# Performance work log

Hardware: AMD Instinct MI355X
Metric: run time of the kernel (lower is better)

Reference implementation:

```python
import jax, jax.numpy as jnp
import numpy as np

# Fixed problem configuration (regularized ragged structure)
B = 8192      # number of trajectories
D = 32        # input_size
H = 128       # hidden_size
PH = 64       # p_hidden
PREP = 10     # prep_hidden
CS = 8        # cov_size
CH = 32       # cov_hidden
NT = 16       # number of observation times
NO = 4096     # observations per time (trajectories observed)
DT = 0.1      # delta_t (1 euler step between consecutive obs times)
NPOST = 4     # euler steps after last observation up to T
LOGC = float(np.log(np.sqrt(2.0 * np.pi)))


def setup_inputs() -> dict:
    key = jax.random.key(0)
    ks = jax.random.split(key, 24)
    f32 = jnp.float32

    def rn(k, shape, fan_in):
        return jax.random.normal(k, shape, f32) / np.sqrt(fan_in)

    X = jax.random.normal(ks[0], (NT, NO, D), f32)
    M = (jax.random.uniform(ks[1], (NT, NO, D)) < 0.7).astype(f32)  # 0/1 observation mask
    # unique trajectory indices per observation time -> deterministic scatter
    obs_idx = jax.vmap(lambda k: jax.random.permutation(k, B)[:NO])(
        jax.random.split(ks[2], NT)).astype(jnp.int32)
    cov = jax.random.normal(ks[3], (B, CS), f32)

    inp = dict(X=X, M=M, obs_idx=obs_idx, cov=cov)
    # covariates_map: Linear(CS,CH) ReLU Linear(CH,H) Tanh
    inp['cm_w1'] = rn(ks[4], (CS, CH), CS);  inp['cm_b1'] = jnp.zeros((CH,), f32)
    inp['cm_w2'] = rn(ks[5], (CH, H), CH);   inp['cm_b2'] = jnp.zeros((H,), f32)
    # p_model: Linear(H,PH) ReLU Linear(PH,2D)
    inp['p_w1'] = rn(ks[6], (H, PH), H);     inp['p_b1'] = jnp.zeros((PH,), f32)
    inp['p_w2'] = rn(ks[7], (PH, 2 * D), PH); inp['p_b2'] = jnp.zeros((2 * D,), f32)
    # GRUODECell with input 2D
    inp['xz_w'] = rn(ks[8], (2 * D, H), 2 * D); inp['xz_b'] = jnp.zeros((H,), f32)
    inp['hz_w'] = rn(ks[9], (H, H), H)
    inp['xn_w'] = rn(ks[10], (2 * D, H), 2 * D); inp['xn_b'] = jnp.zeros((H,), f32)
    inp['hn_w'] = rn(ks[11], (H, H), H)
    # GRUCell(PREP*D, H): stored as [in, 3H] / [H, 3H], chunk order r,z,n
    inp['w_ih'] = rn(ks[12], (PREP * D, 3 * H), PREP * D)
    inp['w_hh'] = rn(ks[13], (H, 3 * H), H)
    inp['b_ih'] = jnp.zeros((3 * H,), f32)
    inp['b_hh'] = jnp.zeros((3 * H,), f32)
    # observation preprocessing
    std = np.sqrt(2.0 / (4 + PREP))
    inp['w_prep'] = std * jax.random.normal(ks[14], (D, 4, PREP), f32)
    inp['bias_prep'] = 0.1 + jnp.zeros((D, PREP), f32)
    return inp


def reference(X, M, obs_idx, cov,
              cm_w1, cm_b1, cm_w2, cm_b2,
              p_w1, p_b1, p_w2, p_b2,
              xz_w, xz_b, hz_w, xn_w, xn_b, hn_w,
              w_ih, w_hh, b_ih, b_hh, w_prep, bias_prep):
    def p_model(h):
        return jax.nn.relu(h @ p_w1 + p_b1) @ p_w2 + p_b2

    def gru_ode(p, h):  # returns dh/dt as in GRUODECell
        z = jax.nn.sigmoid(p @ xz_w + xz_b + h @ hz_w)
        n = jnp.tanh(p @ xn_w + xn_b + (z * h) @ hn_w)
        return (1.0 - z) * (n - h)

    def gru_cell(x, h):  # torch nn.GRUCell semantics, chunks r,z,n
        gi = x @ w_ih + b_ih
        gh = h @ w_hh + b_hh
        ir, iz, inn = jnp.split(gi, 3, axis=1)
        hr, hz, hn = jnp.split(gh, 3, axis=1)
        r = jax.nn.sigmoid(ir + hr)
        z = jax.nn.sigmoid(iz + hz)
        n = jnp.tanh(inn + r * hn)
        return (1.0 - z) * n + z * h

    h = jnp.tanh(jax.nn.relu(cov @ cm_w1 + cm_b1) @ cm_w2 + cm_b2)  # [B,H]
    p = p_model(h)                                                   # [B,2D]
    loss = jnp.float32(0.0)

    for t in range(NT):
        # one euler ODE step up to the observation time
        h = h + DT * gru_ode(p, h)
        p = p_model(h)
        # Bayesian jump at observed trajectories
        idx = obs_idx[t]            # [NO]
        Xo, Mo = X[t], M[t]         # [NO,D]
        po = p[idx]                 # gather [NO,2D]
        mean, logvar = jnp.split(po, 2, axis=1)
        sigma = jnp.exp(0.5 * logvar)
        err = (Xo - mean) / sigma
        loss = loss + (0.5 * ((err ** 2 + logvar + 2.0 * LOGC) * Mo)).sum()
        feats = jnp.stack([Xo, mean, logvar, err], axis=-1)          # [NO,D,4]
        gin = jax.nn.relu(jnp.einsum('ndf,dfp->ndp', feats, w_prep) + bias_prep)
        gin = (gin * Mo[:, :, None]).reshape(NO, D * PREP)
        h = h.at[idx].set(gru_cell(gin, h[idx]))                     # scatter update
        p = p_model(h)

    for _ in range(NPOST):  # evolve to horizon T
        h = h + DT * gru_ode(p, h)
        p = p_model(h)

    return h, p, loss
```

## Files before the change

kernel.cpp:

```cpp
#include <hip/hip_runtime.h>

#define B_     8192
#define D_     32
#define H_     128
#define PH_    64
#define PREP_  10
#define CS_    8
#define CH_    32
#define NT_    16
#define NO_    4096
#define NPOST_ 4
#define DT_    0.1f
#define TWO_LOGC 1.8378770664093453f

#define OFF_XZXN 0
#define OFF_HZ   16384
#define OFF_HN   32768
#define OFF_PW1  49152
#define OFF_PW2  57344
#define OFF_WIH  61440
#define OFF_WHH  184320
#define BLOB_ELEMS 233472
#define INV_BYTE_OFF ((size_t)BLOB_ELEMS*2)
#define WJP_BYTE_OFF (INV_BYTE_OFF + 262144)

#define WL_XZXN 0
#define WL_HZ   16384
#define WL_PW1  32768
#define WL_PW2  40960
#define WL_TOT  45056

#define STRH 136
#define STRP 72
#define STRG 328
#define PFSTR 67

#define SB_XZ    0
#define SB_XN    128
#define SB_P1    256
#define SB_P2    320
#define SB_BRZ   384
#define SB_BIN   640
#define SB_BHN   768
#define SB_TOT   896

typedef float f4  __attribute__((ext_vector_type(4)));
typedef short bf8 __attribute__((ext_vector_type(8)));

__device__ __forceinline__ f4 mfma16(bf8 a, bf8 b, f4 c){
  return __builtin_amdgcn_mfma_f32_16x16x32_bf16(a,b,c,0,0,0);
}
__device__ __forceinline__ unsigned short f2bf(float f){
  unsigned int u = __builtin_bit_cast(unsigned int, f);
  u = (u + 0x7FFFu + ((u>>16)&1u)) >> 16;
  return (unsigned short)u;
}
__device__ __forceinline__ unsigned int cvtpk(float lo, float hi){
  unsigned int r;
  asm("v_cvt_pk_bf16_f32 %0, %1, %2" : "=v"(r) : "v"(lo), "v"(hi));
  return r;
}
__device__ __forceinline__ float sigmoidf_(float x){ return 1.f/(1.f+__expf(-x)); }
__device__ __forceinline__ float tanhf_(float x){
  float e = __expf(2.f*x);
  return 1.f - 2.f/(e+1.f);
}
__device__ __forceinline__ int permk(int k){
  return ((k>>5)<<5) | (((k>>2)&3)<<3) | (((k>>4)&1)<<2) | (k&3);
}

template<int NKC,int NSEL,int NTT,int NRT>
__device__ __forceinline__ void gemmW(f4 (&acc)[NRT][NSEL], const unsigned short* Ald,
                                      int strideUsh, const unsigned short* __restrict__ Bg,
                                      int lane, int tile0){
  const int lc = lane & 15, a4 = lane >> 4;
  const unsigned short* a0 = Ald + lc*strideUsh + a4*8;
  const unsigned short* bl = Bg + (size_t)tile0*512 + lane*8;
  #pragma unroll 2
  for(int kc=0;kc<NKC;kc++){
    bf8 av0 = *(const bf8*)(a0 + kc*32);
    bf8 av1;
    if constexpr(NRT==2) av1 = *(const bf8*)(a0 + 16*strideUsh + kc*32);
    #pragma unroll
    for(int s=0;s<NSEL;s++){
      bf8 bv = *(const bf8*)(bl + (size_t)(kc*NTT + s*8)*512);
      acc[0][s] = mfma16(av0, bv, acc[0][s]);
      if constexpr(NRT==2) acc[1][s] = mfma16(av1, bv, acc[1][s]);
    }
  }
}

__global__ void init_inv(unsigned short* inv, float* outLoss){
  int i = blockIdx.x*256 + threadIdx.x;
  if(i < NT_*B_) inv[i] = 0xFFFFu;
  if(i == 0) *outLoss = 0.f;
}

__global__ void scatter_inv(unsigned short* inv, const int* __restrict__ obs){
  int i = blockIdx.x*256 + threadIdx.x;
  if(i < NT_*NO_){
    int t = i >> 12;
    int o = i & 4095;
    inv[(size_t)t*B_ + obs[i]] = (unsigned short)o;
  }
}

__global__ void build_blobs(const float* __restrict__ pw1, const float* __restrict__ pw2,
                            const float* __restrict__ xzw, const float* __restrict__ xnw,
                            const float* __restrict__ hzw, const float* __restrict__ hnw,
                            const float* __restrict__ wih, const float* __restrict__ whh,
                            const float* __restrict__ wprep, const float* __restrict__ bprep,
                            unsigned short* __restrict__ blob, float* __restrict__ wjp){
  int sec = blockIdx.y;
  int e = blockIdx.x*256 + threadIdx.x;
  if(sec==7){
    if(e < 32*51){
      int d = e/51, r = e%51, pr = r/5, c = r%5;
      float v = 0.f;
      if(pr < PREP_) v = (c<4) ? wprep[d*40 + c*10 + pr] : bprep[d*10 + pr];
      wjp[e] = v;
    }
    return;
  }
  const float* src=nullptr; int N, ld, off, cnt;
  switch(sec){
    case 0: src=nullptr; N=256; ld=0;   off=OFF_XZXN; cnt=16384;  break;
    case 1: src=hzw;  N=128; ld=128; off=OFF_HZ;   cnt=16384;  break;
    case 2: src=hnw;  N=128; ld=128; off=OFF_HN;   cnt=16384;  break;
    case 3: src=pw1;  N=64;  ld=64;  off=OFF_PW1;  cnt=8192;   break;
    case 4: src=pw2;  N=64;  ld=64;  off=OFF_PW2;  cnt=4096;   break;
    case 5: src=wih;  N=384; ld=384; off=OFF_WIH;  cnt=122880; break;
    default:src=whh;  N=384; ld=384; off=OFF_WHH;  cnt=49152;  break;
  }
  if(e >= cnt) return;
  int ntiles = N >> 4;
  int perkc = ntiles << 9;
  int kc = e / perkc, rem = e % perkc;
  int nt = rem >> 9, li = rem & 511;
  int lane = li >> 3, j = li & 7;
  int n = nt*16 + (lane & 15);
  int k = kc*32 + ((lane>>4)&3)*4 + (j&3) + ((j>>2)<<4);
  float v;
  if(sec==0) v = (n<128) ? xzw[(size_t)k*128+n] : xnw[(size_t)k*128 + (n-128)];
  else       v = src[(size_t)k*ld + n];
  blob[off + e] = f2bf(v);
}

__global__ __launch_bounds__(512,2) void fused(
    const float* __restrict__ X, const float* __restrict__ M,
    const float* __restrict__ cov,
    const float* __restrict__ cm_w1, const float* __restrict__ cm_b1,
    const float* __restrict__ cm_w2, const float* __restrict__ cm_b2,
    const float* __restrict__ p_b1, const float* __restrict__ p_b2,
    const float* __restrict__ xz_b, const float* __restrict__ xn_b,
    const float* __restrict__ b_ih, const float* __restrict__ b_hh,
    const unsigned short* __restrict__ blob, const float* __restrict__ wjp,
    const unsigned short* __restrict__ inv,
    float* __restrict__ outH, float* __restrict__ outP, float* __restrict__ outLoss)
{
  __shared__ __align__(16) unsigned short wlds[WL_TOT];
  __shared__ __align__(16) unsigned short hb[32*STRH];
  __shared__ __align__(16) unsigned short pb[32*STRP];
  __shared__ __align__(16) unsigned short un[32*STRG];
  __shared__ __align__(16) float pf32[32*PFSTR];
  __shared__ float sb[SB_TOT];
  __shared__ float sbJ[32*51];
  __shared__ int obsO[32];
  __shared__ float lred[8];

  const int tid  = threadIdx.x;
  const int lane = tid & 63;
  const int w    = tid >> 6;
  const int lc   = lane & 15;
  const int a4   = lane >> 4;
  const int base = blockIdx.x * 32;
  float lsum = 0.f;

  for(int i=tid;i<128;i+=512){ sb[SB_XZ+i]=xz_b[i]; sb[SB_XN+i]=xn_b[i];
                               sb[SB_BIN+i]=b_ih[256+i]; sb[SB_BHN+i]=b_hh[256+i]; }
  for(int i=tid;i<64;i+=512){ sb[SB_P1+i]=p_b1[i]; sb[SB_P2+i]=p_b2[i]; }
  for(int i=tid;i<256;i+=512) sb[SB_BRZ+i]=b_ih[i]+b_hh[i];
  for(int i=tid;i<32*51;i+=512) sbJ[i]=wjp[i];
  for(int i=tid*8;i<32768;i+=4096) *(uint4*)(wlds+i)      = *(const uint4*)(blob+i);
  for(int i=tid*8;i<12288;i+=4096) *(uint4*)(wlds+32768+i)= *(const uint4*)(blob+49152+i);

  {
    float* c1f = pf32;
    float* hInitF = (float*)un;
    int row = tid>>4, q = tid&15;
    float a[2];
    #pragma unroll
    for(int j=0;j<2;j++) a[j]=cm_b1[q*2+j];
    #pragma unroll
    for(int k=0;k<CS_;k++){
      float cv = cov[(size_t)(base+row)*CS_+k];
      #pragma unroll
      for(int j=0;j<2;j++) a[j] += cv*cm_w1[k*CH_+q*2+j];
    }
    #pragma unroll
    for(int j=0;j<2;j++) c1f[row*36+q*2+j] = fmaxf(a[j],0.f);
    __syncthreads();
    float acc2[8];
    #pragma unroll
    for(int j=0;j<8;j++) acc2[j]=cm_b2[q*8+j];
    for(int k=0;k<CH_;k++){
      float cv = c1f[row*36+k];
      #pragma unroll
      for(int j=0;j<8;j++) acc2[j] += cv*cm_w2[k*H_+q*8+j];
    }
    #pragma unroll
    for(int j=0;j<8;j++) hInitF[row*132+q*8+j] = tanhf_(acc2[j]);
    __syncthreads();
  }

  f4 hFr[2];
  f4 pFr;
  const int prt = w & 1, pct = w >> 1;
  {
    float* hInitF = (float*)un;
    #pragma unroll
    for(int rt=0;rt<2;rt++)
      #pragma unroll
      for(int g=0;g<4;g++)
        hFr[rt][g] = hInitF[(rt*16+a4*4+g)*132 + w*16+lc];
    __syncthreads();
    #pragma unroll
    for(int rt=0;rt<2;rt++)
      #pragma unroll
      for(int g=0;g<4;g++)
        hb[(rt*16+a4*4+g)*STRH + permk(w*16+lc)] = f2bf(hFr[rt][g]);
    __syncthreads();
  }

  auto pmodel = [&](){
    f4 acc[1][1];
    { float bv = sb[SB_P1 + pct*16+lc]; f4 t={bv,bv,bv,bv}; acc[0][0]=t; }
    gemmW<4,1,4,1>(acc, hb + prt*16*STRH, STRH, wlds+WL_PW1, lane, pct);
    #pragma unroll
    for(int g=0;g<4;g++)
      un[(prt*16+a4*4+g)*STRP + permk(pct*16+lc)] = f2bf(fmaxf(acc[0][0][g],0.f));
    __syncthreads();
    { float bv = sb[SB_P2 + pct*16+lc]; f4 t={bv,bv,bv,bv}; acc[0][0]=t; }
    gemmW<2,1,4,1>(acc, un + prt*16*STRP, STRP, wlds+WL_PW2, lane, pct);
    pFr = acc[0][0];
    #pragma unroll
    for(int g=0;g<4;g++){
      int row = prt*16+a4*4+g, col = pct*16+lc;
      float v = acc[0][0][g];
      pb[row*STRP + permk(col)] = f2bf(v);
      pf32[row*PFSTR + col] = v;
    }
    __syncthreads();
  };

  auto euler = [&](){
    bf8 hnB[4];
    #pragma unroll
    for(int kc=0;kc<4;kc++)
      hnB[kc] = *(const bf8*)(blob + OFF_HN + (size_t)(kc*8+w)*512 + lane*8);
    f4 ax[2][2];
    #pragma unroll
    for(int rt=0;rt<2;rt++){
      float bz = sb[SB_XZ + w*16+lc], bn = sb[SB_XN + w*16+lc];
      f4 tz={bz,bz,bz,bz}, tn={bn,bn,bn,bn};
      ax[rt][0]=tz; ax[rt][1]=tn;
    }
    gemmW<2,2,16,2>(ax, pb, STRP, wlds+WL_XZXN, lane, w);
    f4 ah[2][1]; { f4 z4={0.f,0.f,0.f,0.f}; ah[0][0]=z4; ah[1][0]=z4; }
    gemmW<4,1,8,2>(ah, hb, STRH, wlds+WL_HZ, lane, w);
    f4 zr[2];
    #pragma unroll
    for(int rt=0;rt<2;rt++)
      #pragma unroll
      for(int g=0;g<4;g++){
        float z = sigmoidf_(ax[rt][0][g] + ah[rt][0][g]);
        zr[rt][g]=z;
        un[(rt*16+a4*4+g)*STRH + permk(w*16+lc)] = f2bf(z*hFr[rt][g]);
      }
    __syncthreads();
    f4 ah2[2]; { f4 z4={0.f,0.f,0.f,0.f}; ah2[0]=z4; ah2[1]=z4; }
    {
      const unsigned short* a0 = un + lc*STRH + a4*8;
      #pragma unroll
      for(int kc=0;kc<4;kc++){
        bf8 av0 = *(const bf8*)(a0 + kc*32);
        bf8 av1 = *(const bf8*)(a0 + 16*STRH + kc*32);
        ah2[0] = mfma16(av0, hnB[kc], ah2[0]);
        ah2[1] = mfma16(av1, hnB[kc], ah2[1]);
      }
    }
    #pragma unroll
    for(int rt=0;rt<2;rt++)
      #pragma unroll
      for(int g=0;g<4;g++){
        float nn = tanhf_(ax[rt][1][g] + ah2[rt][g]);
        float ho = hFr[rt][g];
        float hv = ho + DT_*(1.f-zr[rt][g])*(nn-ho);
        hFr[rt][g]=hv;
        hb[(rt*16+a4*4+g)*STRH + permk(w*16+lc)] = f2bf(hv);
      }
    __syncthreads();
  };

  auto jump = [&](int o0, int o1, float x0, float m0, float x1, float m1){
    {
      int rp = tid>>5, d = tid&31;
      int row0 = rp*2, row1 = rp*2+1;
      if(d==0){ obsO[row0]=o0; obsO[row1]=o1; }
      float mean0 = pf32[row0*PFSTR + d], lv0 = pf32[row0*PFSTR + D_ + d];
      float mean1 = pf32[row1*PFSTR + d], lv1 = pf32[row1*PFSTR + D_ + d];
      float er0 = (x0-mean0)*__expf(-0.5f*lv0);
      float er1 = (x1-mean1)*__expf(-0.5f*lv1);
      lsum += 0.5f*((er0*er0 + lv0 + TWO_LOGC)*m0 + (er1*er1 + lv1 + TWO_LOGC)*m1);
      const float* wj = sbJ + d*51;
      unsigned short* g0 = un + row0*STRG;
      unsigned short* g1 = un + row1*STRG;
      #pragma unroll
      for(int pr=0;pr<PREP_;pr+=2){
        const float* ca = wj + pr*5;
        const float* cb = ca + 5;
        float sa0 = fmaxf(x0*ca[0] + mean0*ca[1] + lv0*ca[2] + er0*ca[3] + ca[4], 0.f)*m0;
        float sb0 = fmaxf(x0*cb[0] + mean0*cb[1] + lv0*cb[2] + er0*cb[3] + cb[4], 0.f)*m0;
        float sa1 = fmaxf(x1*ca[0] + mean1*ca[1] + lv1*ca[2] + er1*ca[3] + ca[4], 0.f)*m1;
        float sb1 = fmaxf(x1*cb[0] + mean1*cb[1] + lv1*cb[2] + er1*cb[3] + cb[4], 0.f)*m1;
        int pos = permk(d*PREP_ + pr);
        *(unsigned int*)(g0 + pos) = cvtpk(sa0, sb0);
        *(unsigned int*)(g1 + pos) = cvtpk(sa1, sb1);
      }
    }
    __syncthreads();
    f4 gi[2][3];
    #pragma unroll
    for(int rt=0;rt<2;rt++){
      float br = sb[SB_BRZ + w*16+lc], bz = sb[SB_BRZ+128 + w*16+lc], bn = sb[SB_BIN + w*16+lc];
      f4 tr={br,br,br,br}, tz={bz,bz,bz,bz}, tn={bn,bn,bn,bn};
      gi[rt][0]=tr; gi[rt][1]=tz; gi[rt][2]=tn;
    }
    gemmW<10,3,24,2>(gi, un, STRG, blob+OFF_WIH, lane, w);
    f4 gh[2][3];
    #pragma unroll
    for(int rt=0;rt<2;rt++){
      float bhn = sb[SB_BHN + w*16+lc];
      f4 z4={0.f,0.f,0.f,0.f}, tn={bhn,bhn,bhn,bhn};
      gh[rt][0]=z4; gh[rt][1]=z4; gh[rt][2]=tn;
    }
    gemmW<4,3,24,2>(gh, hb, STRH, blob+OFF_WHH, lane, w);
    __syncthreads();
    #pragma unroll
    for(int rt=0;rt<2;rt++)
      #pragma unroll
      for(int g=0;g<4;g++){
        int row = rt*16+a4*4+g;
        float r = sigmoidf_(gi[rt][0][g] + gh[rt][0][g]);
        float z = sigmoidf_(gi[rt][1][g] + gh[rt][1][g]);
        float nn = tanhf_(gi[rt][2][g] + r*gh[rt][2][g]);
        float hv = (1.f-z)*nn + z*hFr[rt][g];
        if(obsO[row]>=0){
          hFr[rt][g]=hv;
          hb[row*STRH + permk(w*16+lc)] = f2bf(hv);
        }
      }
    __syncthreads();
  };

  pmodel();
  for(int t=0;t<NT_;t++){
    int rp = tid>>5, d = tid&31;
    unsigned short iv0 = inv[(size_t)t*B_ + base + rp*2];
    unsigned short iv1 = inv[(size_t)t*B_ + base + rp*2 + 1];
    int o0 = (iv0==0xFFFFu)? -1 : (int)iv0;
    int o1 = (iv1==0xFFFFu)? -1 : (int)iv1;
    float x0=0.f,m0=0.f,x1=0.f,m1=0.f;
    if(o0>=0){
      x0 = X[((size_t)t*NO_+o0)*D_ + d];
      m0 = M[((size_t)t*NO_+o0)*D_ + d];
    }
    if(o1>=0){
      x1 = X[((size_t)t*NO_+o1)*D_ + d];
      m1 = M[((size_t)t*NO_+o1)*D_ + d];
    }
    euler();
    pmodel();
    jump(o0, o1, x0, m0, x1, m1);
    pmodel();
  }
  for(int it=0;it<NPOST_;it++){
    euler();
    pmodel();
  }

  #pragma unroll
  for(int rt=0;rt<2;rt++)
    #pragma unroll
    for(int g=0;g<4;g++)
      outH[(size_t)(base + rt*16+a4*4+g)*H_ + w*16+lc] = hFr[rt][g];
  #pragma unroll
  for(int g=0;g<4;g++)
    outP[(size_t)(base + prt*16+a4*4+g)*(2*D_) + pct*16+lc] = pFr[g];

  #pragma unroll
  for(int off=32;off>0;off>>=1) lsum += __shfl_down(lsum, off);
  if(lane==0) lred[w]=lsum;
  __syncthreads();
  if(tid==0){
    float s = 0.f;
    #pragma unroll
    for(int i=0;i<8;i++) s += lred[i];
    atomicAdd(outLoss, s);
  }
}

extern "C" void kernel_launch(void* const* d_in, const int* in_sizes, int n_in,
                              void* d_out, int out_size, void* d_ws, size_t ws_size,
                              hipStream_t stream){
  const float* X      = (const float*)d_in[0];
  const float* M      = (const float*)d_in[1];
  const int*   obs    = (const int*)  d_in[2];
  const float* cov    = (const float*)d_in[3];
  const float* cm_w1  = (const float*)d_in[4];
  const float* cm_b1  = (const float*)d_in[5];
  const float* cm_w2  = (const float*)d_in[6];
  const float* cm_b2  = (const float*)d_in[7];
  const float* p_w1   = (const float*)d_in[8];
  const float* p_b1   = (const float*)d_in[9];
  const float* p_w2   = (const float*)d_in[10];
  const float* p_b2   = (const float*)d_in[11];
  const float* xz_w   = (const float*)d_in[12];
  const float* xz_b   = (const float*)d_in[13];
  const float* hz_w   = (const float*)d_in[14];
  const float* xn_w   = (const float*)d_in[15];
  const float* xn_b   = (const float*)d_in[16];
  const float* hn_w   = (const float*)d_in[17];
  const float* w_ih   = (const float*)d_in[18];
  const float* w_hh   = (const float*)d_in[19];
  const float* b_ih   = (const float*)d_in[20];
  const float* b_hh   = (const float*)d_in[21];
  const float* w_prep = (const float*)d_in[22];
  const float* bprep  = (const float*)d_in[23];

  unsigned short* blob = (unsigned short*)d_ws;
  unsigned short* inv  = (unsigned short*)((char*)d_ws + INV_BYTE_OFF);
  float*          wjp  = (float*)((char*)d_ws + WJP_BYTE_OFF);
  float* outH = (float*)d_out;
  float* outP = outH + (size_t)B_*H_;
  float* outLoss = outP + (size_t)B_*2*D_;

  init_inv   <<<dim3((NT_*B_+255)/256), dim3(256), 0, stream>>>(inv, outLoss);
  scatter_inv<<<dim3((NT_*NO_+255)/256), dim3(256), 0, stream>>>(inv, obs);
  build_blobs<<<dim3(480,8), dim3(256), 0, stream>>>(p_w1,p_w2,xz_w,xn_w,hz_w,hn_w,w_ih,w_hh,
                                                     w_prep,bprep, blob, wjp);
  fused      <<<dim3(B_/32), dim3(512), 0, stream>>>(
      X, M, cov, cm_w1, cm_b1, cm_w2, cm_b2, p_b1, p_b2, xz_b, xn_b,
      b_ih, b_hh, blob, wjp, inv, outH, outP, outLoss);
}
```

Measured before the change: 189.4 us.

## Fold p_model second layer into GRU-ODE input weights to skip p computation

```diff
diff --git a/kernel.cpp b/kernel.cpp
--- a/kernel.cpp
+++ b/kernel.cpp
@@ -110,6 +110,8 @@
                             const float* __restrict__ hzw, const float* __restrict__ hnw,
                             const float* __restrict__ wih, const float* __restrict__ whh,
                             const float* __restrict__ wprep, const float* __restrict__ bprep,
+                            const float* __restrict__ pb2, const float* __restrict__ xzb,
+                            const float* __restrict__ xnb,
                             unsigned short* __restrict__ blob, float* __restrict__ wjp){
   int sec = blockIdx.y;
   int e = blockIdx.x*256 + threadIdx.x;
@@ -119,6 +121,14 @@
       float v = 0.f;
       if(pr < PREP_) v = (c<4) ? wprep[d*40 + c*10 + pr] : bprep[d*10 + pr];
       wjp[e] = v;
+    } else if(e < 32*51 + 256){
+      int n = e - 32*51;
+      float acc = (n<128)? xzb[n] : xnb[n-128];
+      for(int m=0;m<2*D_;m++){
+        float xz = (n<128)? xzw[(size_t)m*H_+n] : xnw[(size_t)m*H_+(n-128)];
+        acc += pb2[m]*xz;
+      }
+      wjp[e] = acc;
     }
     return;
   }
@@ -141,8 +151,16 @@
   int n = nt*16 + (lane & 15);
   int k = kc*32 + ((lane>>4)&3)*4 + (j&3) + ((j>>2)<<4);
   float v;
-  if(sec==0) v = (n<128) ? xzw[(size_t)k*128+n] : xnw[(size_t)k*128 + (n-128)];
-  else       v = src[(size_t)k*ld + n];
+  if(sec==0){
+    float acc = 0.f;
+    #pragma unroll 4
+    for(int m=0;m<2*D_;m++){
+      float xz = (n<128)? xzw[(size_t)m*H_+n] : xnw[(size_t)m*H_+(n-128)];
+      acc += pw2[(size_t)k*(2*D_)+m]*xz;
+    }
+    v = acc;
+  }
+  else v = src[(size_t)k*ld + n];
   blob[off + e] = f2bf(v);
 }
 
@@ -152,7 +170,6 @@
     const float* __restrict__ cm_w1, const float* __restrict__ cm_b1,
     const float* __restrict__ cm_w2, const float* __restrict__ cm_b2,
     const float* __restrict__ p_b1, const float* __restrict__ p_b2,
-    const float* __restrict__ xz_b, const float* __restrict__ xn_b,
     const float* __restrict__ b_ih, const float* __restrict__ b_hh,
     const unsigned short* __restrict__ blob, const float* __restrict__ wjp,
     const unsigned short* __restrict__ inv,
@@ -160,7 +177,7 @@
 {
   __shared__ __align__(16) unsigned short wlds[WL_TOT];
   __shared__ __align__(16) unsigned short hb[32*STRH];
-  __shared__ __align__(16) unsigned short pb[32*STRP];
+  __shared__ __align__(16) unsigned short qb[32*STRP];
   __shared__ __align__(16) unsigned short un[32*STRG];
   __shared__ __align__(16) float pf32[32*PFSTR];
   __shared__ float sb[SB_TOT];
@@ -176,7 +193,8 @@
   const int base = blockIdx.x * 32;
   float lsum = 0.f;
 
-  for(int i=tid;i<128;i+=512){ sb[SB_XZ+i]=xz_b[i]; sb[SB_XN+i]=xn_b[i];
+  const float* fb = wjp + 32*51;
+  for(int i=tid;i<128;i+=512){ sb[SB_XZ+i]=fb[i]; sb[SB_XN+i]=fb[128+i];
                                sb[SB_BIN+i]=b_ih[256+i]; sb[SB_BHN+i]=b_hh[256+i]; }
   for(int i=tid;i<64;i+=512){ sb[SB_P1+i]=p_b1[i]; sb[SB_P2+i]=p_b2[i]; }
   for(int i=tid;i<256;i+=512) sb[SB_BRZ+i]=b_ih[i]+b_hh[i];
@@ -232,24 +250,24 @@
     __syncthreads();
   }
 
-  auto pmodel = [&](){
+  auto qphase = [&](){
     f4 acc[1][1];
     { float bv = sb[SB_P1 + pct*16+lc]; f4 t={bv,bv,bv,bv}; acc[0][0]=t; }
     gemmW<4,1,4,1>(acc, hb + prt*16*STRH, STRH, wlds+WL_PW1, lane, pct);
     #pragma unroll
     for(int g=0;g<4;g++)
-      un[(prt*16+a4*4+g)*STRP + permk(pct*16+lc)] = f2bf(fmaxf(acc[0][0][g],0.f));
-    __syncthreads();
+      qb[(prt*16+a4*4+g)*STRP + permk(pct*16+lc)] = f2bf(fmaxf(acc[0][0][g],0.f));
+    __syncthreads();
+  };
+
+  auto pphase = [&](bool fin){
+    f4 acc[1][1];
     { float bv = sb[SB_P2 + pct*16+lc]; f4 t={bv,bv,bv,bv}; acc[0][0]=t; }
-    gemmW<2,1,4,1>(acc, un + prt*16*STRP, STRP, wlds+WL_PW2, lane, pct);
-    pFr = acc[0][0];
-    #pragma unroll
-    for(int g=0;g<4;g++){
-      int row = prt*16+a4*4+g, col = pct*16+lc;
-      float v = acc[0][0][g];
-      pb[row*STRP + permk(col)] = f2bf(v);
-      pf32[row*PFSTR + col] = v;
-    }
+    gemmW<2,1,4,1>(acc, qb + prt*16*STRP, STRP, wlds+WL_PW2, lane, pct);
+    if(fin) pFr = acc[0][0];
+    #pragma unroll
+    for(int g=0;g<4;g++)
+      pf32[(prt*16+a4*4+g)*PFSTR + pct*16+lc] = acc[0][0][g];
     __syncthreads();
   };
 
@@ -265,7 +283,7 @@
       f4 tz={bz,bz,bz,bz}, tn={bn,bn,bn,bn};
       ax[rt][0]=tz; ax[rt][1]=tn;
     }
-    gemmW<2,2,16,2>(ax, pb, STRP, wlds+WL_XZXN, lane, w);
+    gemmW<2,2,16,2>(ax, qb, STRP, wlds+WL_XZXN, lane, w);
     f4 ah[2][1]; { f4 z4={0.f,0.f,0.f,0.f}; ah[0][0]=z4; ah[1][0]=z4; }
     gemmW<4,1,8,2>(ah, hb, STRH, wlds+WL_HZ, lane, w);
     f4 zr[2];
@@ -363,7 +381,7 @@
     __syncthreads();
   };
 
-  pmodel();
+  qphase();
   for(int t=0;t<NT_;t++){
     int rp = tid>>5, d = tid&31;
     unsigned short iv0 = inv[(size_t)t*B_ + base + rp*2];
@@ -380,14 +398,16 @@
       m1 = M[((size_t)t*NO_+o1)*D_ + d];
     }
     euler();
-    pmodel();
+    qphase();
+    pphase(false);
     jump(o0, o1, x0, m0, x1, m1);
-    pmodel();
+    qphase();
   }
   for(int it=0;it<NPOST_;it++){
     euler();
-    pmodel();
-  }
+    qphase();
+  }
+  pphase(true);
 
   #pragma unroll
   for(int rt=0;rt<2;rt++)
@@ -448,8 +468,8 @@
   init_inv   <<<dim3((NT_*B_+255)/256), dim3(256), 0, stream>>>(inv, outLoss);
   scatter_inv<<<dim3((NT_*NO_+255)/256), dim3(256), 0, stream>>>(inv, obs);
   build_blobs<<<dim3(480,8), dim3(256), 0, stream>>>(p_w1,p_w2,xz_w,xn_w,hz_w,hn_w,w_ih,w_hh,
-                                                     w_prep,bprep, blob, wjp);
+                                                     w_prep,bprep,p_b2,xz_b,xn_b, blob, wjp);
   fused      <<<dim3(B_/32), dim3(512), 0, stream>>>(
-      X, M, cov, cm_w1, cm_b1, cm_w2, cm_b2, p_b1, p_b2, xz_b, xn_b,
+      X, M, cov, cm_w1, cm_b1, cm_w2, cm_b2, p_b1, p_b2,
       b_ih, b_hh, blob, wjp, inv, outH, outP, outLoss);
 }
```

Measured after the change: 187.4 us. No clear change (-1.1%).
